# Kernel optimization log

Measured on AMD Instinct MI355X. Metric: run time of the kernel, lower is better.

## Reference

```python
import jax, jax.numpy as jnp
import numpy as np

N = 100000
E = 1600000
IN_DIM = 128
H = 64
OUT_DIM = 64
EPS = 1e-5


def batch_norm(x, gamma, beta):
    # BatchNorm1d with batch statistics (training-mode normalization, biased var)
    mu = jnp.mean(x, axis=0)
    var = jnp.var(x, axis=0)
    return (x - mu) * jax.lax.rsqrt(var + EPS) * gamma + beta


def gcn_conv(x, src, dst, W, b, n_nodes):
    # PyG GCNConv: add self-loops, symmetric deg^-1/2 normalization, X W, scatter-add, bias
    loop = jnp.arange(n_nodes, dtype=src.dtype)
    s = jnp.concatenate([src, loop])
    d = jnp.concatenate([dst, loop])
    w = jnp.ones(s.shape[0], dtype=x.dtype)
    deg = jax.ops.segment_sum(w, d, num_segments=n_nodes)
    dinv = jnp.where(deg > 0, jax.lax.rsqrt(deg), 0.0)
    norm = dinv[s] * w * dinv[d]                      # [E+N]
    h = x @ W                                         # [N, out]
    msg = h[s] * norm[:, None]                        # [E+N, out]
    out = jax.ops.segment_sum(msg, d, num_segments=n_nodes)
    return out + b


def setup_inputs() -> dict:
    key = jax.random.key(0)
    ks = jax.random.split(key, 12)
    x = jax.random.normal(ks[0], (N, IN_DIM), dtype=jnp.float32)
    edge_index = jax.random.randint(ks[1], (2, E), 0, N, dtype=jnp.int64)
    s = 0.05
    return {
        "x": x,
        "edge_index": edge_index,
        "bn_in_g": jnp.ones((IN_DIM,), jnp.float32),
        "bn_in_b": jnp.zeros((IN_DIM,), jnp.float32),
        "Wp": jax.random.normal(ks[2], (IN_DIM, H), jnp.float32) * s,
        "bp": jnp.zeros((H,), jnp.float32),
        "W1": jax.random.normal(ks[3], (H, H), jnp.float32) * s,
        "b1": jnp.zeros((H,), jnp.float32),
        "bn1_g": jnp.ones((H,), jnp.float32),
        "bn1_b": jnp.zeros((H,), jnp.float32),
        "W2": jax.random.normal(ks[4], (H, OUT_DIM), jnp.float32) * s,
        "b2": jnp.zeros((OUT_DIM,), jnp.float32),
        "bn2_g": jnp.ones((OUT_DIM,), jnp.float32),
        "bn2_b": jnp.zeros((OUT_DIM,), jnp.float32),
    }


def reference(x, edge_index, bn_in_g, bn_in_b, Wp, bp, W1, b1, bn1_g, bn1_b, W2, b2, bn2_g, bn2_b):
    src, dst = edge_index[0], edge_index[1]
    n = x.shape[0]
    h0 = batch_norm(x, bn_in_g, bn_in_b)
    h0 = jax.nn.relu(h0 @ Wp + bp)
    h1 = gcn_conv(h0, src, dst, W1, b1, n)
    h1 = jax.nn.relu(batch_norm(h1, bn1_g, bn1_b))
    # dropout in eval mode: identity
    h2 = gcn_conv(h1, src, dst, W2, b2, n)
    return batch_norm(h2, bn2_g, bn2_b)
```

## Files before the change

### kernel.cpp

```cpp
#include <hip/hip_runtime.h>
#include <hip/hip_bf16.h>

#define EPS 1e-5f

__device__ __forceinline__ void acc_q(float* acc, uint2 v, float s) {
    acc[0] += s * (float)((int)(v.x << 24) >> 24);
    acc[1] += s * (float)((int)(v.x << 16) >> 24);
    acc[2] += s * (float)((int)(v.x << 8) >> 24);
    acc[3] += s * (float)((int)v.x >> 24);
    acc[4] += s * (float)((int)(v.y << 24) >> 24);
    acc[5] += s * (float)((int)(v.y << 16) >> 24);
    acc[6] += s * (float)((int)(v.y << 8) >> 24);
    acc[7] += s * (float)((int)v.y >> 24);
}

__global__ __launch_bounds__(256) void k_pre(const int* __restrict__ dst,
                                             int* __restrict__ cc,
                                             const float* __restrict__ x,
                                             float* __restrict__ xsum,
                                             float* __restrict__ xsq,
                                             int E, int N, int NB) {
    __shared__ float lsf[512];
    int tx = threadIdx.x;
    if (blockIdx.x < 512) {
        int* h = (int*)lsf;
        for (int i = tx; i < NB; i += 256) h[i] = 0;
        __syncthreads();
        int stride = 512 * 256;
        for (int e = blockIdx.x * 256 + tx; e < E; e += stride)
            atomicAdd(&h[dst[e] >> 8], 1);
        __syncthreads();
        for (int i = tx; i < NB; i += 256)
            if (h[i]) atomicAdd(&cc[i], h[i]);
    } else {
        float* ls = lsf;
        float* lq = lsf + 256;
        int b2 = blockIdx.x - 512;
        int col = tx & 127, half = tx >> 7;
        float s = 0.f, q = 0.f;
        for (int r = b2 * 2 + half; r < N; r += 1024) {
            float v = x[(long long)r * 128 + col];
            s += v; q += v * v;
        }
        ls[tx] = s; lq[tx] = q;
        __syncthreads();
        if (half == 0) {
            s = ls[tx] + ls[tx + 128];
            q = lq[tx] + lq[tx + 128];
            atomicAdd(&xsum[col], s);
            atomicAdd(&xsq[col], q);
        }
    }
}

__global__ void k_cscan(const int* __restrict__ cc, int* __restrict__ coff,
                        int* __restrict__ cur, int NB, int E) {
    __shared__ int ls[512];
    int tx = threadIdx.x;
    int v = (tx < NB) ? cc[tx] : 0;
    ls[tx] = v;
    __syncthreads();
    for (int off = 1; off < 512; off <<= 1) {
        int u = (tx >= off) ? ls[tx - off] : 0;
        __syncthreads();
        ls[tx] += u;
        __syncthreads();
    }
    int excl = ls[tx] - v;
    if (tx < NB) { coff[tx] = excl; cur[tx] = excl; }
    if (tx == NB - 1) coff[NB] = excl + v;
}

#define PCHUNK 4096
__global__ __launch_bounds__(256) void k_mid(
    const int* __restrict__ src, const int* __restrict__ dst,
    int* __restrict__ cursor, unsigned* __restrict__ packbuf, int E, int NB, int PB,
    const float* __restrict__ x, const float* __restrict__ stats,
    const float* __restrict__ g, const float* __restrict__ bbn,
    const float* __restrict__ Wp, const float* __restrict__ bp,
    float* __restrict__ H, float invN, int N) {
    __shared__ int h[512], start[520], delta[512];
    __shared__ unsigned buf[PCHUNK];
    int tx = threadIdx.x;
    if (blockIdx.x < PB) {
        int e0 = blockIdx.x * PCHUNK;
        int e1 = min(e0 + PCHUNK, E);
        int csize = e1 - e0;
        h[tx] = 0; h[tx + 256] = 0;
        __syncthreads();
        for (int e = e0 + tx; e < e1; e += 256)
            atomicAdd(&h[dst[e] >> 8], 1);
        __syncthreads();
        start[tx] = h[tx]; start[tx + 256] = h[tx + 256];
        __syncthreads();
        for (int off = 1; off < 512; off <<= 1) {
            int i0 = tx, i1 = tx + 256;
            int v0 = (i0 >= off) ? start[i0 - off] : 0;
            int v1 = (i1 >= off) ? start[i1 - off] : 0;
            __syncthreads();
            start[i0] += v0; start[i1] += v1;
            __syncthreads();
        }
#pragma unroll
        for (int t = 0; t < 2; t++) {
            int b = tx + t * 256;
            int c = h[b];
            int excl = start[b] - c;
            if (b < NB) {
                int gbase = c ? atomicAdd(&cursor[b], c) : 0;
                delta[b] = gbase - excl;
            }
            start[b] = excl;
        }
        __syncthreads();
        h[tx] = start[tx]; h[tx + 256] = start[tx + 256];
        if (tx == 0) start[NB] = csize;
        __syncthreads();
        for (int e = e0 + tx; e < e1; e += 256) {
            int d = dst[e];
            int b = d >> 8;
            int rank = atomicAdd(&h[b], 1);
            buf[rank] = ((unsigned)src[e] << 8) | (unsigned)(d & 255);
        }
        __syncthreads();
        for (int i = tx; i < csize; i += 256) {
            unsigned pk = buf[i];
            int lo = 0, hi = NB;
            while (hi - lo > 1) {
                int mid = (lo + hi) >> 1;
                if (start[mid] <= i) lo = mid; else hi = mid;
            }
            packbuf[delta[lo] + i] = pk;
        }
    } else {
        float* sc = (float*)h;
        float* sh = (float*)delta;
        if (tx < 128) {
            float mu = stats[tx] * invN;
            float var = stats[128 + tx] * invN - mu * mu;
            float s = g[tx] * rsqrtf(var + EPS);
            sc[tx] = s;
            sh[tx] = bbn[tx] - mu * s;
        }
        __syncthreads();
        int r = (blockIdx.x - PB) * 256 + tx;
        if (r >= N) return;
        float acc[64];
#pragma unroll
        for (int j = 0; j < 64; j++) acc[j] = 0.f;
        const float4* x4 = (const float4*)(x + (long long)r * 128);
        for (int c4 = 0; c4 < 32; c4++) {
            float4 xv = x4[c4];
            int cb = c4 * 4;
            xv.x = xv.x * sc[cb + 0] + sh[cb + 0];
            xv.y = xv.y * sc[cb + 1] + sh[cb + 1];
            xv.z = xv.z * sc[cb + 2] + sh[cb + 2];
            xv.w = xv.w * sc[cb + 3] + sh[cb + 3];
#pragma unroll
            for (int q = 0; q < 4; q++) {
                float xs = (q == 0) ? xv.x : (q == 1) ? xv.y : (q == 2) ? xv.z : xv.w;
                const float* wrow = Wp + (c4 * 4 + q) * 64;
#pragma unroll
                for (int j = 0; j < 64; j++) acc[j] += xs * wrow[j];
            }
        }
        float4* out4 = (float4*)(H + (long long)r * 64);
#pragma unroll
        for (int i = 0; i < 16; i++) {
            float4 v;
            v.x = fmaxf(acc[4 * i + 0] + bp[4 * i + 0], 0.f);
            v.y = fmaxf(acc[4 * i + 1] + bp[4 * i + 1], 0.f);
            v.z = fmaxf(acc[4 * i + 2] + bp[4 * i + 2], 0.f);
            v.w = fmaxf(acc[4 * i + 3] + bp[4 * i + 3], 0.f);
            out4[i] = v;
        }
    }
}

__global__ __launch_bounds__(512) void k_build(const unsigned* __restrict__ packbuf,
                                               const int* __restrict__ coff,
                                               int* __restrict__ rowptr,
                                               float* __restrict__ dinv,
                                               int* __restrict__ eidx, int N, int E) {
    __shared__ int cnt[256], loff[256], wsum[4];
    int b = blockIdx.x;
    int tx = threadIdx.x;
    int beg = coff[b], end = coff[b + 1];
    if (tx < 256) cnt[tx] = 0;
    __syncthreads();
    for (int e = beg + tx; e < end; e += 512)
        atomicAdd(&cnt[packbuf[e] & 255u], 1);
    __syncthreads();
    if (tx < 256) {
        int c = cnt[tx];
        int lane = tx & 63, wid = tx >> 6;
        int v = c;
#pragma unroll
        for (int off = 1; off < 64; off <<= 1) {
            int u = __shfl_up(v, off);
            if (lane >= off) v += u;
        }
        if (lane == 63) wsum[wid] = v;
        __syncthreads();
        int wbase = 0;
        for (int w = 0; w < wid; w++) wbase += wsum[w];
        int excl = wbase + v - c;
        loff[tx] = excl;
        int node = b * 256 + tx;
        if (node < N) {
            rowptr[node] = beg + excl;
            dinv[node] = rsqrtf(1.0f + (float)c);
        }
    } else {
        __syncthreads();
    }
    if (b == 0 && tx == 0) rowptr[N] = E;
    __syncthreads();
    for (int e = beg + tx; e < end; e += 512) {
        unsigned pk = packbuf[e];
        int pos = atomicAdd(&loff[pk & 255u], 1);
        eidx[beg + pos] = (int)(pk >> 8);
    }
}

template <bool BNRELU>
__global__ __launch_bounds__(256) void k_gemm_scale(
    const float* __restrict__ In, const float* __restrict__ W,
    const float* __restrict__ dinv, const float* __restrict__ ssum,
    const float* __restrict__ ssq, const float* __restrict__ g,
    const float* __restrict__ bb, float invN, unsigned* __restrict__ Bq,
    float* __restrict__ S, int N) {
    __shared__ float scs[64], shs[64];
    int tx = threadIdx.x;
    if (BNRELU) {
        if (tx < 64) {
            float mu = ssum[tx] * invN;
            float var = ssq[tx] * invN - mu * mu;
            float s = g[tx] * rsqrtf(var + EPS);
            scs[tx] = s;
            shs[tx] = bb[tx] - mu * s;
        }
        __syncthreads();
    }
    int r = blockIdx.x * blockDim.x + tx;
    if (r >= N) return;
    float acc[64];
#pragma unroll
    for (int j = 0; j < 64; j++) acc[j] = 0.f;
    const float4* in4 = (const float4*)(In + (long long)r * 64);
    for (int c4 = 0; c4 < 16; c4++) {
        float4 xv = in4[c4];
        if (BNRELU) {
            int cb = c4 * 4;
            xv.x = fmaxf(xv.x * scs[cb + 0] + shs[cb + 0], 0.f);
            xv.y = fmaxf(xv.y * scs[cb + 1] + shs[cb + 1], 0.f);
            xv.z = fmaxf(xv.z * scs[cb + 2] + shs[cb + 2], 0.f);
            xv.w = fmaxf(xv.w * scs[cb + 3] + shs[cb + 3], 0.f);
        }
#pragma unroll
        for (int q = 0; q < 4; q++) {
            float xs = (q == 0) ? xv.x : (q == 1) ? xv.y : (q == 2) ? xv.z : xv.w;
            const float* wrow = W + (c4 * 4 + q) * 64;
#pragma unroll
            for (int j = 0; j < 64; j++) acc[j] += xs * wrow[j];
        }
    }
    float dv = dinv[r];
    float vmax = 0.f;
#pragma unroll
    for (int j = 0; j < 64; j++) {
        acc[j] *= dv;
        vmax = fmaxf(vmax, fabsf(acc[j]));
    }
    S[r] = vmax * (1.0f / 127.0f);
    float inv = (vmax > 0.f) ? (127.0f / vmax) : 0.f;
    uint4* b4 = (uint4*)(Bq + (long long)r * 16);
#pragma unroll
    for (int i = 0; i < 4; i++) {
        unsigned w[4];
#pragma unroll
        for (int k2 = 0; k2 < 4; k2++) {
            int bsx = i * 16 + k2 * 4;
            unsigned q0 = (unsigned)((int)rintf(acc[bsx + 0] * inv)) & 255u;
            unsigned q1 = (unsigned)((int)rintf(acc[bsx + 1] * inv)) & 255u;
            unsigned q2 = (unsigned)((int)rintf(acc[bsx + 2] * inv)) & 255u;
            unsigned q3 = (unsigned)((int)rintf(acc[bsx + 3] * inv)) & 255u;
            w[k2] = q0 | (q1 << 8) | (q2 << 16) | (q3 << 24);
        }
        b4[i] = make_uint4(w[0], w[1], w[2], w[3]);
    }
}

__global__ __launch_bounds__(256) void k_gather_finish(
    const uint2* __restrict__ B, const float* __restrict__ S,
    const int* __restrict__ rowptr, const int* __restrict__ eidx,
    const float* __restrict__ dinv, const float* __restrict__ bias,
    float* __restrict__ Out, float* __restrict__ ssum, float* __restrict__ ssq, int N) {
    int tx = threadIdx.x;
    int g = tx >> 3;
    int l = tx & 7;
    int d = blockIdx.x * 32 + g;

    float s[8], q[8];
#pragma unroll
    for (int j = 0; j < 8; j++) { s[j] = 0.f; q[j] = 0.f; }

    if (d < N) {
        int beg = rowptr[d], end = rowptr[d + 1];
        float acc[8];
#pragma unroll
        for (int j = 0; j < 8; j++) acc[j] = 0.f;
        {
            uint2 v0 = B[(long long)d * 8 + l];
            acc_q(acc, v0, S[d]);
        }
        int k = beg;
        for (; k + 3 < end; k += 4) {
            int i0 = eidx[k + 0], i1 = eidx[k + 1], i2 = eidx[k + 2], i3 = eidx[k + 3];
            uint2 a0 = B[(long long)i0 * 8 + l];
            uint2 a1 = B[(long long)i1 * 8 + l];
            uint2 a2 = B[(long long)i2 * 8 + l];
            uint2 a3 = B[(long long)i3 * 8 + l];
            float s0 = S[i0], s1 = S[i1], s2 = S[i2], s3 = S[i3];
            acc_q(acc, a0, s0); acc_q(acc, a1, s1);
            acc_q(acc, a2, s2); acc_q(acc, a3, s3);
        }
        for (; k + 1 < end; k += 2) {
            int i0 = eidx[k + 0], i1 = eidx[k + 1];
            uint2 a0 = B[(long long)i0 * 8 + l];
            uint2 a1 = B[(long long)i1 * 8 + l];
            float s0 = S[i0], s1 = S[i1];
            acc_q(acc, a0, s0); acc_q(acc, a1, s1);
        }
        if (k < end) {
            int i0 = eidx[k];
            uint2 a0 = B[(long long)i0 * 8 + l];
            acc_q(acc, a0, S[i0]);
        }
        float dv = dinv[d];
        float4 o0, o1;
#pragma unroll
        for (int j = 0; j < 8; j++) {
            float v = acc[j] * dv + bias[8 * l + j];
            ((j < 4) ? (&o0.x)[j] : (&o1.x)[j - 4]) = v;
            s[j] += v; q[j] += v * v;
        }
        float4* outp = (float4*)(Out + (long long)d * 64 + 8 * l);
        outp[0] = o0;
        outp[1] = o1;
    }

#pragma unroll
    for (int m = 8; m <= 32; m <<= 1) {
#pragma unroll
        for (int j = 0; j < 8; j++) {
            s[j] += __shfl_xor(s[j], m, 64);
            q[j] += __shfl_xor(q[j], m, 64);
        }
    }
    __shared__ float ws_s[4][64], ws_q[4][64];
    int wv = tx >> 6, ln = tx & 63;
    if (ln < 8) {
#pragma unroll
        for (int j = 0; j < 8; j++) {
            ws_s[wv][ln * 8 + j] = s[j];
            ws_q[wv][ln * 8 + j] = q[j];
        }
    }
    __syncthreads();
    if (tx < 64) {
        float S2 = ws_s[0][tx] + ws_s[1][tx] + ws_s[2][tx] + ws_s[3][tx];
        float Q2 = ws_q[0][tx] + ws_q[1][tx] + ws_q[2][tx] + ws_q[3][tx];
        atomicAdd(&ssum[tx], S2);
        atomicAdd(&ssq[tx], Q2);
    }
}

__global__ __launch_bounds__(256) void k_final(const float* __restrict__ In,
                                               const float* __restrict__ ssum,
                                               const float* __restrict__ ssq,
                                               const float* __restrict__ g,
                                               const float* __restrict__ bb, float invN,
                                               float* __restrict__ out, int total4) {
    __shared__ float scs[64], shs[64];
    int tx = threadIdx.x;
    if (tx < 64) {
        float mu = ssum[tx] * invN;
        float var = ssq[tx] * invN - mu * mu;
        float s = g[tx] * rsqrtf(var + EPS);
        scs[tx] = s;
        shs[tx] = bb[tx] - mu * s;
    }
    __syncthreads();
    int t = blockIdx.x * blockDim.x + tx;
    if (t < total4) {
        float4 v = ((const float4*)In)[t];
        int j = (t * 4) & 63;
        v.x = v.x * scs[j + 0] + shs[j + 0];
        v.y = v.y * scs[j + 1] + shs[j + 1];
        v.z = v.z * scs[j + 2] + shs[j + 2];
        v.w = v.w * scs[j + 3] + shs[j + 3];
        ((float4*)out)[t] = v;
    }
}

extern "C" void kernel_launch(void* const* d_in, const int* in_sizes, int n_in,
                              void* d_out, int out_size, void* d_ws, size_t ws_size,
                              hipStream_t stream) {
    const float* x       = (const float*)d_in[0];
    const int*   ei      = (const int*)d_in[1];
    const float* bn_in_g = (const float*)d_in[2];
    const float* bn_in_b = (const float*)d_in[3];
    const float* Wp      = (const float*)d_in[4];
    const float* bp      = (const float*)d_in[5];
    const float* W1      = (const float*)d_in[6];
    const float* b1      = (const float*)d_in[7];
    const float* bn1_g   = (const float*)d_in[8];
    const float* bn1_b   = (const float*)d_in[9];
    const float* W2      = (const float*)d_in[10];
    const float* b2      = (const float*)d_in[11];
    const float* bn2_g   = (const float*)d_in[12];
    const float* bn2_b   = (const float*)d_in[13];

    int N = in_sizes[0] / 128;
    int E = in_sizes[1] / 2;
    const int* src = ei;
    const int* dst = ei + E;
    int NB = (N + 255) >> 8;

    long long Npad = ((long long)N + 128) & ~127LL;
    int*   cc     = (int*)d_ws;
    float* stats  = (float*)(cc + 512);
    int*   coff   = (int*)(stats + 512);
    int*   cur    = coff + 640;
    int*   rowptr = cur + 512;
    float* dinv   = (float*)(rowptr + Npad);
    float* S      = dinv + Npad;
    unsigned* packbuf = (unsigned*)(S + Npad);
    int*   eidx   = (int*)(packbuf + ((E + 127) & ~127));
    unsigned* Bq  = (unsigned*)(eidx + ((E + 127) & ~127));
    float* H      = (float*)d_out;

    int nb = (N + 255) / 256;
    int gb = (N + 31) / 32;
    int PB = (E + PCHUNK - 1) / PCHUNK;
    float invN = 1.0f / (float)N;

    hipMemsetAsync(d_ws, 0, (512 + 512) * 4, stream);

    k_pre<<<1024, 256, 0, stream>>>(dst, cc, x, stats, stats + 128, E, N, NB);
    k_cscan<<<1, 512, 0, stream>>>(cc, coff, cur, NB, E);
    k_mid<<<PB + nb, 256, 0, stream>>>(src, dst, cur, packbuf, E, NB, PB,
                                       x, stats, bn_in_g, bn_in_b, Wp, bp, H, invN, N);
    k_build<<<NB, 512, 0, stream>>>(packbuf, coff, rowptr, dinv, eidx, N, E);

    k_gemm_scale<false><<<nb, 256, 0, stream>>>(H, W1, dinv, nullptr, nullptr, nullptr,
                                                nullptr, invN, Bq, S, N);
    k_gather_finish<<<gb, 256, 0, stream>>>((const uint2*)Bq, S, rowptr, eidx, dinv,
                                            b1, H, stats + 256, stats + 320, N);

    k_gemm_scale<true><<<nb, 256, 0, stream>>>(H, W2, dinv, stats + 256, stats + 320,
                                               bn1_g, bn1_b, invN, Bq, S, N);
    k_gather_finish<<<gb, 256, 0, stream>>>((const uint2*)Bq, S, rowptr, eidx, dinv,
                                            b2, H, stats + 384, stats + 448, N);

    k_final<<<(N * 16 + 255) / 256, 256, 0, stream>>>(H, stats + 384, stats + 448,
                                                      bn2_g, bn2_b, invN, H, N * 16);
}
```

Before: 483.2 us.

## Replace CSR build with bucket-level LDS atomic aggregation in gather

Drops the per-node CSR construction kernel (rowptr/eidx) and keeps only the 128-node bucket partition of edges. The gather kernel now processes one bucket per block, accumulating messages into a 128x64 float LDS tile with shared-memory atomics instead of per-destination register sums. A lightweight degree kernel replaces the build step, and bucket size shrinks from 256 to 128 nodes, with the scans rewritten as wave-shuffle scans. This removes a full edge pass and scatter, but adds eight LDS float atomics per edge element and uses 32KB of LDS per gather block, which may limit occupancy.

```diff
diff --git a/kernel.cpp b/kernel.cpp
--- a/kernel.cpp
+++ b/kernel.cpp
@@ -3,15 +3,14 @@
 
 #define EPS 1e-5f
 
-__device__ __forceinline__ void acc_q(float* acc, uint2 v, float s) {
-    acc[0] += s * (float)((int)(v.x << 24) >> 24);
-    acc[1] += s * (float)((int)(v.x << 16) >> 24);
-    acc[2] += s * (float)((int)(v.x << 8) >> 24);
-    acc[3] += s * (float)((int)v.x >> 24);
-    acc[4] += s * (float)((int)(v.y << 24) >> 24);
-    acc[5] += s * (float)((int)(v.y << 16) >> 24);
-    acc[6] += s * (float)((int)(v.y << 8) >> 24);
-    acc[7] += s * (float)((int)v.y >> 24);
+__device__ __forceinline__ float q2f(uint2 a, int j) {
+    unsigned w = (j < 4) ? a.x : a.y;
+    int sh = (j & 3) * 8;
+    return (float)((int)(w << (24 - sh)) >> 24);
+}
+__device__ __forceinline__ void lds_add8(float* base, uint2 a, float s) {
+#pragma unroll
+    for (int j = 0; j < 8; j++) atomicAdd(base + j, s * q2f(a, j));
 }
 
 __global__ __launch_bounds__(256) void k_pre(const int* __restrict__ dst,
@@ -20,21 +19,20 @@
                                              float* __restrict__ xsum,
                                              float* __restrict__ xsq,
                                              int E, int N, int NB) {
-    __shared__ float lsf[512];
+    __shared__ int h[1024];
     int tx = threadIdx.x;
     if (blockIdx.x < 512) {
-        int* h = (int*)lsf;
-        for (int i = tx; i < NB; i += 256) h[i] = 0;
+        for (int i = tx; i < 1024; i += 256) h[i] = 0;
         __syncthreads();
         int stride = 512 * 256;
         for (int e = blockIdx.x * 256 + tx; e < E; e += stride)
-            atomicAdd(&h[dst[e] >> 8], 1);
+            atomicAdd(&h[dst[e] >> 7], 1);
         __syncthreads();
         for (int i = tx; i < NB; i += 256)
             if (h[i]) atomicAdd(&cc[i], h[i]);
     } else {
-        float* ls = lsf;
-        float* lq = lsf + 256;
+        float* ls = (float*)h;
+        float* lq = ls + 256;
         int b2 = blockIdx.x - 512;
         int col = tx & 127, half = tx >> 7;
         float s = 0.f, q = 0.f;
@@ -55,20 +53,32 @@
 
 __global__ void k_cscan(const int* __restrict__ cc, int* __restrict__ coff,
                         int* __restrict__ cur, int NB, int E) {
-    __shared__ int ls[512];
+    __shared__ int wsum[4];
     int tx = threadIdx.x;
-    int v = (tx < NB) ? cc[tx] : 0;
-    ls[tx] = v;
-    __syncthreads();
-    for (int off = 1; off < 512; off <<= 1) {
-        int u = (tx >= off) ? ls[tx - off] : 0;
-        __syncthreads();
-        ls[tx] += u;
-        __syncthreads();
-    }
-    int excl = ls[tx] - v;
-    if (tx < NB) { coff[tx] = excl; cur[tx] = excl; }
-    if (tx == NB - 1) coff[NB] = excl + v;
+    int b0 = tx * 4;
+    int cs[4];
+#pragma unroll
+    for (int i = 0; i < 4; i++) cs[i] = cc[b0 + i];
+    int tsum = cs[0] + cs[1] + cs[2] + cs[3];
+    int lane = tx & 63, wid = tx >> 6;
+    int v = tsum;
+#pragma unroll
+    for (int off = 1; off < 64; off <<= 1) {
+        int u = __shfl_up(v, off);
+        if (lane >= off) v += u;
+    }
+    if (lane == 63) wsum[wid] = v;
+    __syncthreads();
+    int wbase = 0;
+    for (int w = 0; w < wid; w++) wbase += wsum[w];
+    int run = wbase + v - tsum;
+#pragma unroll
+    for (int i = 0; i < 4; i++) {
+        int idx = b0 + i;
+        if (idx < NB) { coff[idx] = run; cur[idx] = run; }
+        run += cs[i];
+    }
+    if (tx == 0) coff[NB] = E;
 }
 
 #define PCHUNK 4096
@@ -79,48 +89,54 @@
     const float* __restrict__ g, const float* __restrict__ bbn,
     const float* __restrict__ Wp, const float* __restrict__ bp,
     float* __restrict__ H, float invN, int N) {
-    __shared__ int h[512], start[520], delta[512];
+    __shared__ int h[1024], start[1028], delta[1024], wsc[4];
     __shared__ unsigned buf[PCHUNK];
     int tx = threadIdx.x;
     if (blockIdx.x < PB) {
         int e0 = blockIdx.x * PCHUNK;
         int e1 = min(e0 + PCHUNK, E);
         int csize = e1 - e0;
-        h[tx] = 0; h[tx + 256] = 0;
+        for (int i = tx; i < 1024; i += 256) h[i] = 0;
         __syncthreads();
         for (int e = e0 + tx; e < e1; e += 256)
-            atomicAdd(&h[dst[e] >> 8], 1);
-        __syncthreads();
-        start[tx] = h[tx]; start[tx + 256] = h[tx + 256];
-        __syncthreads();
-        for (int off = 1; off < 512; off <<= 1) {
-            int i0 = tx, i1 = tx + 256;
-            int v0 = (i0 >= off) ? start[i0 - off] : 0;
-            int v1 = (i1 >= off) ? start[i1 - off] : 0;
-            __syncthreads();
-            start[i0] += v0; start[i1] += v1;
-            __syncthreads();
-        }
-#pragma unroll
-        for (int t = 0; t < 2; t++) {
-            int b = tx + t * 256;
-            int c = h[b];
-            int excl = start[b] - c;
-            if (b < NB) {
-                int gbase = c ? atomicAdd(&cursor[b], c) : 0;
-                delta[b] = gbase - excl;
+            atomicAdd(&h[dst[e] >> 7], 1);
+        __syncthreads();
+        int b0 = tx * 4;
+        int cs[4];
+#pragma unroll
+        for (int i = 0; i < 4; i++) cs[i] = h[b0 + i];
+        int tsum = cs[0] + cs[1] + cs[2] + cs[3];
+        int lane = tx & 63, wid = tx >> 6;
+        int v = tsum;
+#pragma unroll
+        for (int off = 1; off < 64; off <<= 1) {
+            int u = __shfl_up(v, off);
+            if (lane >= off) v += u;
+        }
+        if (lane == 63) wsc[wid] = v;
+        __syncthreads();
+        int wbase = 0;
+        for (int w = 0; w < wid; w++) wbase += wsc[w];
+        int run = wbase + v - tsum;
+#pragma unroll
+        for (int i = 0; i < 4; i++) {
+            int idx = b0 + i;
+            start[idx] = run;
+            if (idx < NB && cs[i] > 0) {
+                int gb = atomicAdd(&cursor[idx], cs[i]);
+                delta[idx] = gb - run;
             }
-            start[b] = excl;
-        }
-        __syncthreads();
-        h[tx] = start[tx]; h[tx + 256] = start[tx + 256];
+            run += cs[i];
+        }
+        __syncthreads();
+        for (int i = tx; i < 1024; i += 256) h[i] = start[i];
         if (tx == 0) start[NB] = csize;
         __syncthreads();
         for (int e = e0 + tx; e < e1; e += 256) {
             int d = dst[e];
-            int b = d >> 8;
+            int b = d >> 7;
             int rank = atomicAdd(&h[b], 1);
-            buf[rank] = ((unsigned)src[e] << 8) | (unsigned)(d & 255);
+            buf[rank] = ((unsigned)src[e] << 7) | (unsigned)(d & 127);
         }
         __syncthreads();
         for (int i = tx; i < csize; i += 256) {
@@ -167,60 +183,29 @@
         float4* out4 = (float4*)(H + (long long)r * 64);
 #pragma unroll
         for (int i = 0; i < 16; i++) {
-            float4 v;
-            v.x = fmaxf(acc[4 * i + 0] + bp[4 * i + 0], 0.f);
-            v.y = fmaxf(acc[4 * i + 1] + bp[4 * i + 1], 0.f);
-            v.z = fmaxf(acc[4 * i + 2] + bp[4 * i + 2], 0.f);
-            v.w = fmaxf(acc[4 * i + 3] + bp[4 * i + 3], 0.f);
-            out4[i] = v;
-        }
-    }
-}
-
-__global__ __launch_bounds__(512) void k_build(const unsigned* __restrict__ packbuf,
-                                               const int* __restrict__ coff,
-                                               int* __restrict__ rowptr,
-                                               float* __restrict__ dinv,
-                                               int* __restrict__ eidx, int N, int E) {
-    __shared__ int cnt[256], loff[256], wsum[4];
-    int b = blockIdx.x;
-    int tx = threadIdx.x;
+            float4 vv;
+            vv.x = fmaxf(acc[4 * i + 0] + bp[4 * i + 0], 0.f);
+            vv.y = fmaxf(acc[4 * i + 1] + bp[4 * i + 1], 0.f);
+            vv.z = fmaxf(acc[4 * i + 2] + bp[4 * i + 2], 0.f);
+            vv.w = fmaxf(acc[4 * i + 3] + bp[4 * i + 3], 0.f);
+            out4[i] = vv;
+        }
+    }
+}
+
+__global__ __launch_bounds__(256) void k_deg(const unsigned* __restrict__ packbuf,
+                                             const int* __restrict__ coff,
+                                             float* __restrict__ dinv, int N) {
+    __shared__ int cnt[128];
+    int b = blockIdx.x, tx = threadIdx.x;
+    if (tx < 128) cnt[tx] = 0;
+    __syncthreads();
     int beg = coff[b], end = coff[b + 1];
-    if (tx < 256) cnt[tx] = 0;
-    __syncthreads();
-    for (int e = beg + tx; e < end; e += 512)
-        atomicAdd(&cnt[packbuf[e] & 255u], 1);
-    __syncthreads();
-    if (tx < 256) {
-        int c = cnt[tx];
-        int lane = tx & 63, wid = tx >> 6;
-        int v = c;
-#pragma unroll
-        for (int off = 1; off < 64; off <<= 1) {
-            int u = __shfl_up(v, off);
-            if (lane >= off) v += u;
-        }
-        if (lane == 63) wsum[wid] = v;
-        __syncthreads();
-        int wbase = 0;
-        for (int w = 0; w < wid; w++) wbase += wsum[w];
-        int excl = wbase + v - c;
-        loff[tx] = excl;
-        int node = b * 256 + tx;
-        if (node < N) {
-            rowptr[node] = beg + excl;
-            dinv[node] = rsqrtf(1.0f + (float)c);
-        }
-    } else {
-        __syncthreads();
-    }
-    if (b == 0 && tx == 0) rowptr[N] = E;
-    __syncthreads();
-    for (int e = beg + tx; e < end; e += 512) {
-        unsigned pk = packbuf[e];
-        int pos = atomicAdd(&loff[pk & 255u], 1);
-        eidx[beg + pos] = (int)(pk >> 8);
-    }
+    for (int e = beg + tx; e < end; e += 256)
+        atomicAdd(&cnt[packbuf[e] & 127u], 1);
+    __syncthreads();
+    int node = b * 128 + tx;
+    if (tx < 128 && node < N) dinv[node] = rsqrtf(1.0f + (float)cnt[tx]);
 }
 
 template <bool BNRELU>
@@ -293,78 +278,75 @@
 
 __global__ __launch_bounds__(256) void k_gather_finish(
     const uint2* __restrict__ B, const float* __restrict__ S,
-    const int* __restrict__ rowptr, const int* __restrict__ eidx,
+    const unsigned* __restrict__ packbuf, const int* __restrict__ coff,
     const float* __restrict__ dinv, const float* __restrict__ bias,
     float* __restrict__ Out, float* __restrict__ ssum, float* __restrict__ ssq, int N) {
-    int tx = threadIdx.x;
-    int g = tx >> 3;
-    int l = tx & 7;
-    int d = blockIdx.x * 32 + g;
-
-    float s[8], q[8];
-#pragma unroll
-    for (int j = 0; j < 8; j++) { s[j] = 0.f; q[j] = 0.f; }
-
-    if (d < N) {
-        int beg = rowptr[d], end = rowptr[d + 1];
-        float acc[8];
-#pragma unroll
-        for (int j = 0; j < 8; j++) acc[j] = 0.f;
-        {
-            uint2 v0 = B[(long long)d * 8 + l];
-            acc_q(acc, v0, S[d]);
-        }
-        int k = beg;
-        for (; k + 3 < end; k += 4) {
-            int i0 = eidx[k + 0], i1 = eidx[k + 1], i2 = eidx[k + 2], i3 = eidx[k + 3];
-            uint2 a0 = B[(long long)i0 * 8 + l];
-            uint2 a1 = B[(long long)i1 * 8 + l];
-            uint2 a2 = B[(long long)i2 * 8 + l];
-            uint2 a3 = B[(long long)i3 * 8 + l];
-            float s0 = S[i0], s1 = S[i1], s2 = S[i2], s3 = S[i3];
-            acc_q(acc, a0, s0); acc_q(acc, a1, s1);
-            acc_q(acc, a2, s2); acc_q(acc, a3, s3);
-        }
-        for (; k + 1 < end; k += 2) {
-            int i0 = eidx[k + 0], i1 = eidx[k + 1];
-            uint2 a0 = B[(long long)i0 * 8 + l];
-            uint2 a1 = B[(long long)i1 * 8 + l];
-            float s0 = S[i0], s1 = S[i1];
-            acc_q(acc, a0, s0); acc_q(acc, a1, s1);
-        }
-        if (k < end) {
-            int i0 = eidx[k];
-            uint2 a0 = B[(long long)i0 * 8 + l];
-            acc_q(acc, a0, S[i0]);
-        }
-        float dv = dinv[d];
-        float4 o0, o1;
+    __shared__ float accL[8192];
+    __shared__ float ws_s[4][64], ws_q[4][64];
+    int tx = threadIdx.x, b = blockIdx.x;
+    int g = tx >> 3, l = tx & 7;
+    for (int i = tx; i < 8192; i += 256) accL[i] = 0.f;
+    __syncthreads();
+    int ebeg = coff[b], eend = coff[b + 1];
+    int e = ebeg + g;
+    for (; e + 96 < eend; e += 128) {
+        unsigned p0 = packbuf[e], p1 = packbuf[e + 32], p2 = packbuf[e + 64], p3 = packbuf[e + 96];
+        int s0 = p0 >> 7, s1 = p1 >> 7, s2 = p2 >> 7, s3 = p3 >> 7;
+        uint2 a0 = B[s0 * 8 + l];
+        uint2 a1 = B[s1 * 8 + l];
+        uint2 a2 = B[s2 * 8 + l];
+        uint2 a3 = B[s3 * 8 + l];
+        float f0 = S[s0], f1 = S[s1], f2 = S[s2], f3 = S[s3];
+        lds_add8(&accL[(p0 & 127u) * 64 + l * 8], a0, f0);
+        lds_add8(&accL[(p1 & 127u) * 64 + l * 8], a1, f1);
+        lds_add8(&accL[(p2 & 127u) * 64 + l * 8], a2, f2);
+        lds_add8(&accL[(p3 & 127u) * 64 + l * 8], a3, f3);
+    }
+    for (; e < eend; e += 32) {
+        unsigned p0 = packbuf[e];
+        int s0 = p0 >> 7;
+        uint2 a0 = B[s0 * 8 + l];
+        float f0 = S[s0];
+        lds_add8(&accL[(p0 & 127u) * 64 + l * 8], a0, f0);
+    }
+    __syncthreads();
+    float sS[8], sQ[8];
+#pragma unroll
+    for (int j = 0; j < 8; j++) { sS[j] = 0.f; sQ[j] = 0.f; }
+#pragma unroll
+    for (int t = 0; t < 4; t++) {
+        int ln = g + 32 * t;
+        int d = b * 128 + ln;
+        if (d < N) {
+            uint2 a = B[d * 8 + l];
+            float sv = S[d];
+            float dv = dinv[d];
+            float4 o0, o1;
+#pragma unroll
+            for (int j = 0; j < 8; j++) {
+                float val = (accL[ln * 64 + l * 8 + j] + sv * q2f(a, j)) * dv + bias[l * 8 + j];
+                ((j < 4) ? (&o0.x)[j] : (&o1.x)[j - 4]) = val;
+                sS[j] += val; sQ[j] += val * val;
+            }
+            float4* op = (float4*)(Out + (long long)d * 64 + l * 8);
+            op[0] = o0;
+            op[1] = o1;
+        }
+    }
+#pragma unroll
+    for (int m = 8; m <= 32; m <<= 1) {
 #pragma unroll
         for (int j = 0; j < 8; j++) {
-            float v = acc[j] * dv + bias[8 * l + j];
-            ((j < 4) ? (&o0.x)[j] : (&o1.x)[j - 4]) = v;
-            s[j] += v; q[j] += v * v;
-        }
-        float4* outp = (float4*)(Out + (long long)d * 64 + 8 * l);
-        outp[0] = o0;
-        outp[1] = o1;
-    }
-
-#pragma unroll
-    for (int m = 8; m <= 32; m <<= 1) {
+            sS[j] += __shfl_xor(sS[j], m, 64);
+            sQ[j] += __shfl_xor(sQ[j], m, 64);
+        }
+    }
+    int wv = tx >> 6, ln2 = tx & 63;
+    if (ln2 < 8) {
 #pragma unroll
         for (int j = 0; j < 8; j++) {
-            s[j] += __shfl_xor(s[j], m, 64);
-            q[j] += __shfl_xor(q[j], m, 64);
-        }
-    }
-    __shared__ float ws_s[4][64], ws_q[4][64];
-    int wv = tx >> 6, ln = tx & 63;
-    if (ln < 8) {
-#pragma unroll
-        for (int j = 0; j < 8; j++) {
-            ws_s[wv][ln * 8 + j] = s[j];
-            ws_q[wv][ln * 8 + j] = q[j];
+            ws_s[wv][ln2 * 8 + j] = sS[j];
+            ws_q[wv][ln2 * 8 + j] = sQ[j];
         }
     }
     __syncthreads();
@@ -426,42 +408,39 @@
     int E = in_sizes[1] / 2;
     const int* src = ei;
     const int* dst = ei + E;
-    int NB = (N + 255) >> 8;
+    int NB = (N + 127) >> 7;
 
     long long Npad = ((long long)N + 128) & ~127LL;
     int*   cc     = (int*)d_ws;
-    float* stats  = (float*)(cc + 512);
+    float* stats  = (float*)(cc + 1024);
     int*   coff   = (int*)(stats + 512);
-    int*   cur    = coff + 640;
-    int*   rowptr = cur + 512;
-    float* dinv   = (float*)(rowptr + Npad);
+    int*   cur    = coff + 1056;
+    float* dinv   = (float*)(cur + 1024);
     float* S      = dinv + Npad;
     unsigned* packbuf = (unsigned*)(S + Npad);
-    int*   eidx   = (int*)(packbuf + ((E + 127) & ~127));
-    unsigned* Bq  = (unsigned*)(eidx + ((E + 127) & ~127));
+    unsigned* Bq  = (unsigned*)(packbuf + ((E + 127) & ~127));
     float* H      = (float*)d_out;
 
     int nb = (N + 255) / 256;
-    int gb = (N + 31) / 32;
     int PB = (E + PCHUNK - 1) / PCHUNK;
     float invN = 1.0f / (float)N;
 
-    hipMemsetAsync(d_ws, 0, (512 + 512) * 4, stream);
+    hipMemsetAsync(d_ws, 0, (1024 + 512) * 4, stream);
 
     k_pre<<<1024, 256, 0, stream>>>(dst, cc, x, stats, stats + 128, E, N, NB);
-    k_cscan<<<1, 512, 0, stream>>>(cc, coff, cur, NB, E);
+    k_cscan<<<1, 256, 0, stream>>>(cc, coff, cur, NB, E);
     k_mid<<<PB + nb, 256, 0, stream>>>(src, dst, cur, packbuf, E, NB, PB,
                                        x, stats, bn_in_g, bn_in_b, Wp, bp, H, invN, N);
-    k_build<<<NB, 512, 0, stream>>>(packbuf, coff, rowptr, dinv, eidx, N, E);
+    k_deg<<<NB, 256, 0, stream>>>(packbuf, coff, dinv, N);
 
     k_gemm_scale<false><<<nb, 256, 0, stream>>>(H, W1, dinv, nullptr, nullptr, nullptr,
                                                 nullptr, invN, Bq, S, N);
-    k_gather_finish<<<gb, 256, 0, stream>>>((const uint2*)Bq, S, rowptr, eidx, dinv,
+    k_gather_finish<<<NB, 256, 0, stream>>>((const uint2*)Bq, S, packbuf, coff, dinv,
                                             b1, H, stats + 256, stats + 320, N);
 
     k_gemm_scale<true><<<nb, 256, 0, stream>>>(H, W2, dinv, stats + 256, stats + 320,
                                                bn1_g, bn1_b, invN, Bq, S, N);
-    k_gather_finish<<<gb, 256, 0, stream>>>((const uint2*)Bq, S, rowptr, eidx, dinv,
+    k_gather_finish<<<NB, 256, 0, stream>>>((const uint2*)Bq, S, packbuf, coff, dinv,
                                             b2, H, stats + 384, stats + 448, N);
 
     k_final<<<(N * 16 + 255) / 256, 256, 0, stream>>>(H, stats + 384, stats + 448,
```

Result: slower. 1.672 ms (+246.0%).
